# Performance work log

Hardware: AMD Instinct MI355X
Metric: run time of the kernel (lower is better)

Reference implementation:

```python
import jax, jax.numpy as jnp
import numpy as np

N_NODES = 50000
N_EDGES = 1250000
D_NODE = 64
D_EDGE = 16
D_HID = 64


def setup_inputs() -> dict:
    key = jax.random.key(0)
    ks = jax.random.split(key, 12)

    def lin(k, din, dout):
        kw, kb = jax.random.split(k)
        # lecun_normal-style init (flax Linear default kernel init)
        w = jax.random.normal(kw, (din, dout), dtype=jnp.float32) / np.sqrt(din)
        b = jnp.zeros((dout,), dtype=jnp.float32)
        return w, b

    node_features = jax.random.normal(ks[0], (N_NODES, D_NODE), dtype=jnp.float32)
    edge_features = jax.random.normal(ks[1], (N_EDGES, D_EDGE), dtype=jnp.float32)
    edge_index = jax.random.randint(ks[2], (2, N_EDGES), 0, N_NODES, dtype=jnp.int64 if jax.config.jax_enable_x64 else jnp.int32)

    w_m1, b_m1 = lin(ks[3], D_NODE + D_EDGE, D_HID)
    w_m2, b_m2 = lin(ks[4], D_HID, D_HID)
    w_u1, b_u1 = lin(ks[5], D_NODE + D_HID, D_HID)
    w_u2, b_u2 = lin(ks[6], D_HID, D_HID)

    return {
        "node_features": node_features,
        "edge_features": edge_features,
        "edge_index": edge_index,
        "w_m1": w_m1, "b_m1": b_m1,
        "w_m2": w_m2, "b_m2": b_m2,
        "w_u1": w_u1, "b_u1": b_u1,
        "w_u2": w_u2, "b_u2": b_u2,
    }


def reference(node_features, edge_features, edge_index,
              w_m1, b_m1, w_m2, b_m2, w_u1, b_u1, w_u2, b_u2):
    num_nodes = node_features.shape[0]
    src, dst = edge_index[0], edge_index[1]

    # gather source node features per edge: [E, D_NODE]
    source_features = node_features[src]
    # message MLP: [E, D_NODE+D_EDGE] -> relu -> [E, D_HID]
    msg_in = jnp.concatenate([source_features, edge_features], axis=-1)
    messages = jax.nn.relu(msg_in @ w_m1 + b_m1) @ w_m2 + b_m2

    # sum aggregation to destination nodes: [N, D_HID]
    aggregated = jax.ops.segment_sum(messages, dst, num_segments=num_nodes)

    # update MLP: [N, D_NODE+D_HID] -> relu -> [N, D_HID]
    upd_in = jnp.concatenate([node_features, aggregated], axis=-1)
    return jax.nn.relu(upd_in @ w_u1 + b_u1) @ w_u2 + b_u2
```

## Files before the change

kernel.cpp:

```cpp
#include <hip/hip_runtime.h>
#include <cstdio>


typedef _Float16 f16;
typedef f16  f16x8 __attribute__((ext_vector_type(8)));
typedef f16  f16x4 __attribute__((ext_vector_type(4)));
typedef float f32x4 __attribute__((ext_vector_type(4)));

#define MFMA16(a, b, c) __builtin_amdgcn_mfma_f32_16x16x32_f16(a, b, c, 0, 0, 0)

__global__ void conv_features(const float* __restrict__ x,
                              f16* __restrict__ xh, f16* __restrict__ xl,
                              int n4) {
    int i = blockIdx.x * blockDim.x + threadIdx.x;
    if (i >= n4) return;
    float4 v = ((const float4*)x)[i];
    float vv[4] = {v.x, v.y, v.z, v.w};
    f16x4 hi, lo;
    #pragma unroll
    for (int j = 0; j < 4; ++j) {
        f16 h = (f16)vv[j];
        hi[j] = h;
        lo[j] = (f16)(vv[j] - (float)h);
    }
    ((f16x4*)xh)[i] = hi;
    ((f16x4*)xl)[i] = lo;
}

__global__ void conv_weights(const float* __restrict__ w1,
                             const float* __restrict__ w2,
                             f16* __restrict__ w1th, f16* __restrict__ w1tl,
                             f16* __restrict__ w2th, f16* __restrict__ w2tl) {
    int idx = blockIdx.x * blockDim.x + threadIdx.x;
    if (idx < 64 * 96) {
        int c = idx / 96, k = idx % 96;
        float v = (k < 80) ? w1[k * 64 + c] : 0.f;
        f16 h = (f16)v;
        w1th[c * 96 + k] = h;
        w1tl[c * 96 + k] = (f16)(v - (float)h);
    } else if (idx < 64 * 96 + 64 * 64) {
        int t = idx - 64 * 96;
        int c = t / 64, k = t % 64;
        float v = w2[k * 64 + c];
        f16 h = (f16)v;
        w2th[c * 64 + k] = h;
        w2tl[c * 64 + k] = (f16)(v - (float)h);
    }
}

__global__ __launch_bounds__(256)
void GraphMessagePassing_5952824672257_kernel(
    const f16* __restrict__ nh, const f16* __restrict__ nl,
    const float* __restrict__ edgef,
    const int*  __restrict__ eidx,
    const f16* __restrict__ w1th, const f16* __restrict__ w1tl,
    const f16* __restrict__ w2th, const f16* __restrict__ w2tl,
    const float* __restrict__ b1, const float* __restrict__ b2,
    float* __restrict__ agg, int n_edges, int n_nodes)
{
    __shared__ f16 Hhi[64 * 72];
    __shared__ f16 Hlo[64 * 72];

    const int lane = threadIdx.x & 63;
    const int wid  = threadIdx.x >> 6;
    const int r16  = lane & 15;
    const int g    = lane >> 4;
    const long base = (long)blockIdx.x * 64 + wid * 16;

    long es = base + r16;
    if (es >= n_edges) es = n_edges - 1;
    int s = eidx[es];
    if ((unsigned)s >= (unsigned)n_nodes) s = 0;

    int  dstv[4];
    bool val[4];
    #pragma unroll
    for (int reg = 0; reg < 4; ++reg) {
        long ee = base + g * 4 + reg;
        val[reg] = ee < n_edges;
        long ec = val[reg] ? ee : n_edges - 1;
        int d = eidx[(size_t)n_edges + ec];
        if ((unsigned)d >= (unsigned)n_nodes) d = 0;
        dstv[reg] = d;
    }

    f32x4 acc[4] = {{0.f,0.f,0.f,0.f},{0.f,0.f,0.f,0.f},
                    {0.f,0.f,0.f,0.f},{0.f,0.f,0.f,0.f}};

    #pragma unroll
    for (int kt = 0; kt < 2; ++kt) {
        const int k0 = kt * 32 + g * 8;
        f16x8 ahi = *(const f16x8*)&nh[(size_t)s * 64 + k0];
        f16x8 alo = *(const f16x8*)&nl[(size_t)s * 64 + k0];
        #pragma unroll
        for (int nt = 0; nt < 4; ++nt) {
            const int c = nt * 16 + r16;
            f16x8 bhi = *(const f16x8*)&w1th[c * 96 + k0];
            f16x8 blo = *(const f16x8*)&w1tl[c * 96 + k0];
            acc[nt] = MFMA16(ahi, bhi, acc[nt]);
            acc[nt] = MFMA16(ahi, blo, acc[nt]);
            acc[nt] = MFMA16(alo, bhi, acc[nt]);
        }
    }
    {
        f16x8 ahi = {}; f16x8 alo = {};
        if (g < 2) {
            const float* ep = edgef + (size_t)es * 16 + g * 8;
            float4 v0 = *(const float4*)(ep);
            float4 v1 = *(const float4*)(ep + 4);
            float xv[8] = {v0.x, v0.y, v0.z, v0.w, v1.x, v1.y, v1.z, v1.w};
            #pragma unroll
            for (int j = 0; j < 8; ++j) {
                f16 h = (f16)xv[j];
                ahi[j] = h;
                alo[j] = (f16)(xv[j] - (float)h);
            }
        }
        const int k0 = 64 + g * 8;
        #pragma unroll
        for (int nt = 0; nt < 4; ++nt) {
            const int c = nt * 16 + r16;
            f16x8 bhi = *(const f16x8*)&w1th[c * 96 + k0];
            f16x8 blo = *(const f16x8*)&w1tl[c * 96 + k0];
            acc[nt] = MFMA16(ahi, bhi, acc[nt]);
            acc[nt] = MFMA16(ahi, blo, acc[nt]);
            acc[nt] = MFMA16(alo, bhi, acc[nt]);
        }
    }

    const int ebase = wid * 16 + g * 4;
    #pragma unroll
    for (int nt = 0; nt < 4; ++nt) {
        const int ch = nt * 16 + r16;
        const float bv = b1[ch];
        #pragma unroll
        for (int reg = 0; reg < 4; ++reg) {
            float h = fmaxf(acc[nt][reg] + bv, 0.f);
            f16 hh = (f16)h;
            Hhi[(ebase + reg) * 72 + ch] = hh;
            Hlo[(ebase + reg) * 72 + ch] = (f16)(h - (float)hh);
        }
    }
    __syncthreads();

    f32x4 acc2[4] = {{0.f,0.f,0.f,0.f},{0.f,0.f,0.f,0.f},
                     {0.f,0.f,0.f,0.f},{0.f,0.f,0.f,0.f}};
    const int arow = wid * 16 + r16;
    #pragma unroll
    for (int kt = 0; kt < 2; ++kt) {
        const int k0 = kt * 32 + g * 8;
        f16x8 ahi = *(const f16x8*)&Hhi[arow * 72 + k0];
        f16x8 alo = *(const f16x8*)&Hlo[arow * 72 + k0];
        #pragma unroll
        for (int nt = 0; nt < 4; ++nt) {
            const int c = nt * 16 + r16;
            f16x8 bhi = *(const f16x8*)&w2th[c * 64 + k0];
            f16x8 blo = *(const f16x8*)&w2tl[c * 64 + k0];
            acc2[nt] = MFMA16(ahi, bhi, acc2[nt]);
            acc2[nt] = MFMA16(ahi, blo, acc2[nt]);
            acc2[nt] = MFMA16(alo, bhi, acc2[nt]);
        }
    }

    #pragma unroll
    for (int nt = 0; nt < 4; ++nt) {
        const int ch = nt * 16 + r16;
        const float bv = b2[ch];
        #pragma unroll
        for (int reg = 0; reg < 4; ++reg) {
            if (val[reg])
                atomicAdd(agg + (size_t)dstv[reg] * 64 + ch,
                          acc2[nt][reg] + bv);
        }
    }
}

#define TPB 256

__global__ __launch_bounds__(TPB)
void node_mlp_coop(
    const float* __restrict__ nodef,
    const float* __restrict__ agg,
    const float* __restrict__ w1,
    const float* __restrict__ b1,
    const float* __restrict__ w2,
    const float* __restrict__ b2,
    float* __restrict__ out,
    int n_nodes)
{
    __shared__ float HB[64][65];
    float* __restrict__ Xf = &HB[0][0];

    const int tid  = threadIdx.x;
    const int lane = tid & 63;
    const int wch  = __builtin_amdgcn_readfirstlane(tid >> 6) * 16;

    const long base = (long)blockIdx.x * 64;

    const int r  = tid & 15;
    const int e0 = tid >> 4;
    size_t rows[4];
    #pragma unroll
    for (int i = 0; i < 4; ++i) {
        long row = base + e0 + i * 16;
        if (row >= n_nodes) row = n_nodes - 1;
        if (row < 0) row = 0;
        rows[i] = (size_t)row * 64;
    }

    float h[16];
    #pragma unroll
    for (int c = 0; c < 16; ++c) h[c] = b1[wch + c];

    float pf[4];
    #pragma unroll
    for (int i = 0; i < 4; ++i) pf[i] = nodef[rows[i] + r];
    #pragma unroll
    for (int i = 0; i < 4; ++i) Xf[r * 66 + e0 + i * 16] = pf[i];
    #pragma unroll
    for (int i = 0; i < 4; ++i) pf[i] = nodef[rows[i] + 16 + r];
    __syncthreads();

    #pragma unroll
    for (int kc = 0; kc < 8; ++kc) {
        const int cur = kc & 1;
        #pragma unroll 4
        for (int r2 = 0; r2 < 16; ++r2) {
            const float xk = Xf[cur * 1056 + r2 * 66 + lane];
            const float* __restrict__ wr = w1 + (kc * 16 + r2) * 64 + wch;
            #pragma unroll
            for (int c = 0; c < 16; ++c) h[c] = fmaf(xk, wr[c], h[c]);
        }
        if (kc < 7) {
            #pragma unroll
            for (int i = 0; i < 4; ++i)
                Xf[(cur ^ 1) * 1056 + r * 66 + e0 + i * 16] = pf[i];
            if (kc < 6) {
                const float* __restrict__ src = (kc + 2 < 4) ? nodef : agg;
                const int ko = ((kc + 2) & 3) * 16;
                #pragma unroll
                for (int i = 0; i < 4; ++i) pf[i] = src[rows[i] + ko + r];
            }
            __syncthreads();
        }
    }
    __syncthreads();

    #pragma unroll
    for (int c = 0; c < 16; ++c) HB[lane][wch + c] = fmaxf(h[c], 0.f);
    __syncthreads();

    float m[16];
    #pragma unroll
    for (int c = 0; c < 16; ++c) m[c] = b2[wch + c];
    #pragma unroll 4
    for (int t = 0; t < 64; ++t) {
        const float xt = HB[lane][t];
        const float* __restrict__ wr = w2 + t * 64 + wch;
        #pragma unroll
        for (int c = 0; c < 16; ++c) m[c] = fmaf(xt, wr[c], m[c]);
    }
    __syncthreads();

    #pragma unroll
    for (int c = 0; c < 16; ++c) HB[lane][wch + c] = m[c];
    __syncthreads();

    const int oc  = lane & 15;
    const int er4 = lane >> 4;
    #pragma unroll
    for (int g = 0; g < 16; ++g) {
        const int le = g * 4 + er4;
        const float v = HB[le][wch + oc];
        if (base + le < n_nodes)
            out[(size_t)(base + le) * 64 + wch + oc] = v;
    }
}

extern "C" void kernel_launch(void* const* d_in, const int* in_sizes, int n_in,
                              void* d_out, int out_size, void* d_ws, size_t ws_size,
                              hipStream_t stream) {
    const float* nodef = (const float*)d_in[0];
    const float* edgef = (const float*)d_in[1];
    const int*   eidx  = (const int*)d_in[2];
    const float* w_m1  = (const float*)d_in[3];
    const float* b_m1  = (const float*)d_in[4];
    const float* w_m2  = (const float*)d_in[5];
    const float* b_m2  = (const float*)d_in[6];
    const float* w_u1  = (const float*)d_in[7];
    const float* b_u1  = (const float*)d_in[8];
    const float* w_u2  = (const float*)d_in[9];
    const float* b_u2  = (const float*)d_in[10];
    float* out = (float*)d_out;

    const int n_nodes = out_size / 64;
    const int n_edges = in_sizes[2] / 2;
    if (n_edges <= 0 || n_nodes <= 0) return;

    char* wsb = (char*)d_ws;
    float* agg = (float*)wsb;
    size_t o = ((size_t)n_nodes * 64 * 4 + 255) & ~(size_t)255;
    f16* nh = (f16*)(wsb + o); o += (size_t)n_nodes * 64 * 2;
    f16* nl = (f16*)(wsb + o); o += (size_t)n_nodes * 64 * 2;
    f16* w1th = (f16*)(wsb + o); o += 64 * 96 * 2;
    f16* w1tl = (f16*)(wsb + o); o += 64 * 96 * 2;
    f16* w2th = (f16*)(wsb + o); o += 64 * 64 * 2;
    f16* w2tl = (f16*)(wsb + o); o += 64 * 64 * 2;

    fprintf(stderr, "[KL] mfma-f16split E=%d N=%d ws=%zu used=%zu\n",
            n_edges, n_nodes, ws_size, o);
    fflush(stderr);

    hipMemsetAsync(agg, 0, (size_t)n_nodes * 64 * sizeof(float), stream);

    const int n4 = n_nodes * 64 / 4;
    conv_features<<<(n4 + 255) / 256, 256, 0, stream>>>(nodef, nh, nl, n4);
    conv_weights<<<(64 * 96 + 64 * 64 + 255) / 256, 256, 0, stream>>>(
        w_m1, w_m2, w1th, w1tl, w2th, w2tl);

    const int blocks_e = (n_edges + 63) / 64;
    GraphMessagePassing_5952824672257_kernel<<<blocks_e, 256, 0, stream>>>(
        nh, nl, edgef, eidx, w1th, w1tl, w2th, w2tl, b_m1, b_m2,
        agg, n_edges, n_nodes);

    const int blocks_n = (n_nodes + 63) / 64;
    node_mlp_coop<<<blocks_n, TPB, 0, stream>>>(
        nodef, agg, w_u1, b_u1, w_u2, b_u2, out, n_nodes);

    hipError_t le = hipGetLastError();
    fprintf(stderr, "[KL] last=%d(%s)\n", (int)le, hipGetErrorName(le));
    fflush(stderr);
}
```

Baseline: 532.4 us.

## Sort edges by destination and segment-reduce messages before atomic accumulation

Adds a per-call counting sort of edges by destination node: a histogram, a three-kernel prefix scan and an atomic placement pass that write sorted src, dst and edge-id arrays. The message kernel reads edges in sorted order, gathers edge features through the edge-id indirection, and stages its outputs in shared memory. Each wave then reduces runs of equal destinations over its 16 edges before issuing float atomics, aiming to cut atomic traffic on the aggregation buffer by roughly the average run length. In exchange it adds several extra launches, integer atomics, scattered writes, and random rather than sequential edge-feature reads.

```diff
diff --git a/kernel.cpp b/kernel.cpp
--- a/kernel.cpp
+++ b/kernel.cpp
@@ -48,18 +48,94 @@
     }
 }
 
+__global__ void hist_k(const int* __restrict__ dst, int* __restrict__ cnt,
+                       int E, int N) {
+    for (int e = blockIdx.x * blockDim.x + threadIdx.x; e < E;
+         e += gridDim.x * blockDim.x) {
+        int d = dst[e];
+        if ((unsigned)d >= (unsigned)N) d = 0;
+        atomicAdd(&cnt[d], 1);
+    }
+}
+
+__global__ void scan_part(const int* __restrict__ cnt, int* __restrict__ part,
+                          int N) {
+    __shared__ int sh[256];
+    const int b = blockIdx.x, t = threadIdx.x;
+    const int end = min((b + 1) * 1024, N);
+    int s = 0;
+    for (int i = b * 1024 + t; i < end; i += 256) s += cnt[i];
+    sh[t] = s;
+    __syncthreads();
+    for (int st = 128; st > 0; st >>= 1) {
+        if (t < st) sh[t] += sh[t + st];
+        __syncthreads();
+    }
+    if (t == 0) part[b] = sh[0];
+}
+
+__global__ void scan_top(int* part, int nb) {
+    if (blockIdx.x == 0 && threadIdx.x == 0) {
+        int run = 0;
+        for (int i = 0; i < nb; ++i) { int v = part[i]; part[i] = run; run += v; }
+    }
+}
+
+__global__ void scan_fin(const int* __restrict__ cnt, const int* __restrict__ part,
+                         int* __restrict__ offs, int N) {
+    __shared__ int sh[256];
+    const int b = blockIdx.x, t = threadIdx.x;
+    const int i0 = b * 1024 + t * 4;
+    int v[4]; int s = 0;
+    #pragma unroll
+    for (int j = 0; j < 4; ++j) {
+        int idx = i0 + j;
+        v[j] = (idx < N) ? cnt[idx] : 0;
+        s += v[j];
+    }
+    sh[t] = s;
+    __syncthreads();
+    for (int st = 1; st < 256; st <<= 1) {
+        int a = (t >= st) ? sh[t - st] : 0;
+        __syncthreads();
+        sh[t] += a;
+        __syncthreads();
+    }
+    int run = sh[t] - s + part[b];
+    #pragma unroll
+    for (int j = 0; j < 4; ++j) {
+        int idx = i0 + j;
+        if (idx < N) offs[idx] = run;
+        run += v[j];
+    }
+}
+
+__global__ void place_k(const int* __restrict__ eidx, int* __restrict__ offs,
+                        int* __restrict__ ssrc, int* __restrict__ sdst,
+                        int* __restrict__ seid, int E, int N) {
+    int e = blockIdx.x * blockDim.x + threadIdx.x;
+    if (e >= E) return;
+    int d = eidx[(size_t)E + e]; if ((unsigned)d >= (unsigned)N) d = 0;
+    int s = eidx[e];             if ((unsigned)s >= (unsigned)N) s = 0;
+    int p = atomicAdd(&offs[d], 1);
+    ssrc[p] = s; sdst[p] = d; seid[p] = e;
+}
+
 __global__ __launch_bounds__(256)
 void GraphMessagePassing_5952824672257_kernel(
     const f16* __restrict__ nh, const f16* __restrict__ nl,
     const float* __restrict__ edgef,
-    const int*  __restrict__ eidx,
+    const int* __restrict__ ssrc, const int* __restrict__ sdst,
+    const int* __restrict__ seid,
     const f16* __restrict__ w1th, const f16* __restrict__ w1tl,
     const f16* __restrict__ w2th, const f16* __restrict__ w2tl,
     const float* __restrict__ b1, const float* __restrict__ b2,
     float* __restrict__ agg, int n_edges, int n_nodes)
 {
-    __shared__ f16 Hhi[64 * 72];
-    __shared__ f16 Hlo[64 * 72];
+    __shared__ __align__(16) char smem[18432];
+    f16*   Hhi = (f16*)smem;
+    f16*   Hlo = (f16*)(smem + 9216);
+    float* F   = (float*)smem;
 
     const int lane = threadIdx.x & 63;
     const int wid  = threadIdx.x >> 6;
@@ -69,24 +145,11 @@
 
     long es = base + r16;
     if (es >= n_edges) es = n_edges - 1;
-    int s = eidx[es];
-    if ((unsigned)s >= (unsigned)n_nodes) s = 0;
-
-    int  dstv[4];
-    bool val[4];
-    #pragma unroll
-    for (int reg = 0; reg < 4; ++reg) {
-        long ee = base + g * 4 + reg;
-        val[reg] = ee < n_edges;
-        long ec = val[reg] ? ee : n_edges - 1;
-        int d = eidx[(size_t)n_edges + ec];
-        if ((unsigned)d >= (unsigned)n_nodes) d = 0;
-        dstv[reg] = d;
-    }
+    const int s   = ssrc[es];
+    const int eid = seid[es];
 
     f32x4 acc[4] = {{0.f,0.f,0.f,0.f},{0.f,0.f,0.f,0.f},
                     {0.f,0.f,0.f,0.f},{0.f,0.f,0.f,0.f}};
-
     #pragma unroll
     for (int kt = 0; kt < 2; ++kt) {
         const int k0 = kt * 32 + g * 8;
@@ -105,7 +168,7 @@
     {
         f16x8 ahi = {}; f16x8 alo = {};
         if (g < 2) {
-            const float* ep = edgef + (size_t)es * 16 + g * 8;
+            const float* ep = edgef + (size_t)eid * 16 + g * 8;
             float4 v0 = *(const float4*)(ep);
             float4 v1 = *(const float4*)(ep + 4);
             float xv[8] = {v0.x, v0.y, v0.z, v0.w, v1.x, v1.y, v1.z, v1.w};
@@ -161,32 +224,43 @@
             acc2[nt] = MFMA16(alo, bhi, acc2[nt]);
         }
     }
+    __syncthreads();
 
     #pragma unroll
     for (int nt = 0; nt < 4; ++nt) {
         const int ch = nt * 16 + r16;
         const float bv = b2[ch];
         #pragma unroll
-        for (int reg = 0; reg < 4; ++reg) {
-            if (val[reg])
-                atomicAdd(agg + (size_t)dstv[reg] * 64 + ch,
-                          acc2[nt][reg] + bv);
-        }
-    }
+        for (int reg = 0; reg < 4; ++reg)
+            F[(ebase + reg) * 68 + ch] = acc2[nt][reg] + bv;
+    }
+
+    const int c = lane;
+    long e0c = (base < n_edges) ? base : (long)n_edges - 1;
+    int curd = sdst[e0c];
+    float accv = 0.f;
+    #pragma unroll 1
+    for (int i = 0; i < 16; ++i) {
+        const long ee = base + i;
+        const bool v = ee < n_edges;
+        const int dnew = v ? sdst[ee] : curd;
+        if (dnew != curd) {
+            atomicAdd(agg + (size_t)curd * 64 + c, accv);
+            accv = 0.f; curd = dnew;
+        }
+        if (v) accv += F[(wid * 16 + i) * 68 + c];
+    }
+    atomicAdd(agg + (size_t)curd * 64 + c, accv);
 }
 
 #define TPB 256
 
 __global__ __launch_bounds__(TPB)
 void node_mlp_coop(
-    const float* __restrict__ nodef,
-    const float* __restrict__ agg,
-    const float* __restrict__ w1,
-    const float* __restrict__ b1,
-    const float* __restrict__ w2,
-    const float* __restrict__ b2,
-    float* __restrict__ out,
-    int n_nodes)
+    const float* __restrict__ nodef, const float* __restrict__ agg,
+    const float* __restrict__ w1, const float* __restrict__ b1,
+    const float* __restrict__ w2, const float* __restrict__ b2,
+    float* __restrict__ out, int n_nodes)
 {
     __shared__ float HB[64][65];
     float* __restrict__ Xf = &HB[0][0];
@@ -194,7 +268,6 @@
     const int tid  = threadIdx.x;
     const int lane = tid & 63;
     const int wch  = __builtin_amdgcn_readfirstlane(tid >> 6) * 16;
-
     const long base = (long)blockIdx.x * 64;
 
     const int r  = tid & 15;
@@ -298,30 +371,46 @@
     if (n_edges <= 0 || n_nodes <= 0) return;
 
     char* wsb = (char*)d_ws;
-    float* agg = (float*)wsb;
-    size_t o = ((size_t)n_nodes * 64 * 4 + 255) & ~(size_t)255;
-    f16* nh = (f16*)(wsb + o); o += (size_t)n_nodes * 64 * 2;
-    f16* nl = (f16*)(wsb + o); o += (size_t)n_nodes * 64 * 2;
-    f16* w1th = (f16*)(wsb + o); o += 64 * 96 * 2;
-    f16* w1tl = (f16*)(wsb + o); o += 64 * 96 * 2;
-    f16* w2th = (f16*)(wsb + o); o += 64 * 64 * 2;
-    f16* w2tl = (f16*)(wsb + o); o += 64 * 64 * 2;
-
-    fprintf(stderr, "[KL] mfma-f16split E=%d N=%d ws=%zu used=%zu\n",
+    size_t o = 0;
+    float* agg = (float*)wsb;           o += ((size_t)n_nodes * 64 * 4 + 255) & ~(size_t)255;
+    f16* nh   = (f16*)(wsb + o);        o += (size_t)n_nodes * 64 * 2;
+    f16* nl   = (f16*)(wsb + o);        o += (size_t)n_nodes * 64 * 2;
+    f16* w1th = (f16*)(wsb + o);        o += 64 * 96 * 2;
+    f16* w1tl = (f16*)(wsb + o);        o += 64 * 96 * 2;
+    f16* w2th = (f16*)(wsb + o);        o += 64 * 64 * 2;
+    f16* w2tl = (f16*)(wsb + o);        o += 64 * 64 * 2;
+    o = (o + 255) & ~(size_t)255;
+    int* cnt  = (int*)(wsb + o);        o += (size_t)n_nodes * 4;
+    int* offs = (int*)(wsb + o);        o += (size_t)n_nodes * 4;
+    int* part = (int*)(wsb + o);        o += 4096;
+    int* ssrc = (int*)(wsb + o);        o += (size_t)n_edges * 4;
+    int* sdst = (int*)(wsb + o);        o += (size_t)n_edges * 4;
+    int* seid = (int*)(wsb + o);        o += (size_t)n_edges * 4;
+
+    fprintf(stderr, "[KL] mfma+sorted-seg E=%d N=%d ws=%zu used=%zu\n",
             n_edges, n_nodes, ws_size, o);
     fflush(stderr);
 
     hipMemsetAsync(agg, 0, (size_t)n_nodes * 64 * sizeof(float), stream);
+    hipMemsetAsync(cnt, 0, (size_t)n_nodes * sizeof(int), stream);
 
     const int n4 = n_nodes * 64 / 4;
     conv_features<<<(n4 + 255) / 256, 256, 0, stream>>>(nodef, nh, nl, n4);
     conv_weights<<<(64 * 96 + 64 * 64 + 255) / 256, 256, 0, stream>>>(
         w_m1, w_m2, w1th, w1tl, w2th, w2tl);
 
+    const int nb = (n_nodes + 1023) / 1024;
+    hist_k<<<1024, 256, 0, stream>>>(eidx + n_edges, cnt, n_edges, n_nodes);
+    scan_part<<<nb, 256, 0, stream>>>(cnt, part, n_nodes);
+    scan_top<<<1, 64, 0, stream>>>(part, nb);
+    scan_fin<<<nb, 256, 0, stream>>>(cnt, part, offs, n_nodes);
+    place_k<<<(n_edges + 255) / 256, 256, 0, stream>>>(
+        eidx, offs, ssrc, sdst, seid, n_edges, n_nodes);
+
     const int blocks_e = (n_edges + 63) / 64;
     GraphMessagePassing_5952824672257_kernel<<<blocks_e, 256, 0, stream>>>(
-        nh, nl, edgef, eidx, w1th, w1tl, w2th, w2tl, b_m1, b_m2,
-        agg, n_edges, n_nodes);
+        nh, nl, edgef, ssrc, sdst, seid, w1th, w1tl, w2th, w2tl,
+        b_m1, b_m2, agg, n_edges, n_nodes);
 
     const int blocks_n = (n_nodes + 63) / 64;
     node_mlp_coop<<<blocks_n, TPB, 0, stream>>>(
```

Measured after the change: 633.4 us. 1.19x slower.
